# Optimization experiments

Measured on AMD Instinct MI355X. Metric: run time of the kernel, lower is better.

The kernel has to match this reference:

```python
import jax, jax.numpy as jnp
import numpy as np

N = 80000      # rechits per event
K = 512        # max truth objects (t_idx in [-1, K))
C = 2          # n_ccoords
NCLS = 6       # pred_id width
Q_MIN = 0.1
S_B = 1.0
NOISE_SCALER = 1.0
BETA_LOSS_SCALE = 1.0
POTENTIAL_SCALING = 1.0
REPULSION_SCALING = 1.0
ENERGY_LOSS_WEIGHT = 1.0
POSITION_LOSS_WEIGHT = 1.0
TIMING_LOSS_WEIGHT = 1.0
CLASSIFICATION_LOSS_WEIGHT = 1.0
CC_DAMPING = 0.001
EPS = 1e-9


def huber(x, d):
    absx = jnp.abs(x)
    return jnp.where(absx < d, x ** 2, d ** 2 + 2.0 * d * (absx - d))


def softclip(x, startclipat):
    x = x / startclipat
    x = jnp.where(x > 1.0, jnp.log(x + 1.0), x)
    return x * startclipat


def calc_energy_weights(t_energy):
    lower_cut = 0.5
    w = jnp.where(t_energy > 10.0, 1.0, (t_energy - lower_cut) / 10.0 * 10.0 / (10.0 - lower_cut))
    return jax.nn.relu(w)


def calc_energy_loss(t_energy, pred_energy):
    # alt_energy_loss=True branch: mild-gradient modified 1-exp form
    ediff = jnp.abs(t_energy - pred_energy)
    l = 10.0 * jnp.exp(-0.1 * ediff ** 2) + 0.01 * ediff
    return softclip(l, 10.0)


def calc_position_loss(t_pos, pred_pos):
    d2 = jnp.sum((t_pos - pred_pos) ** 2, axis=-1, keepdims=True)
    ploss = huber(jnp.sqrt(d2 / 10.0 ** 2 + 0.01), 10.0)
    return softclip(ploss, 3.0)


def calc_timing_loss(t_time, pred_time):
    return softclip(huber(t_time - pred_time, 2.0), 6.0)


def calc_classification_loss(t_pid, pred_id):
    return 1e-08 * jnp.mean(pred_id ** 2, axis=-1, keepdims=True)


def setup_inputs() -> dict:
    key = jax.random.key(0)
    ks = jax.random.split(key, 11)
    t_idx = jax.random.randint(ks[6], (N, 1), 0, K + 1) - 1  # -1 == noise
    return {
        'pred_beta': jax.random.uniform(ks[0], (N, 1), jnp.float32, 0.01, 0.99),
        'pred_ccoords': jax.random.normal(ks[1], (N, C), jnp.float32),
        'pred_energy': 100.0 * jax.random.uniform(ks[2], (N, 1), jnp.float32),
        'pred_pos': jax.random.normal(ks[3], (N, 2), jnp.float32),
        'pred_time': jax.random.normal(ks[4], (N, 1), jnp.float32),
        'pred_id': jax.random.normal(ks[5], (N, NCLS), jnp.float32),
        't_idx': t_idx.astype(jnp.int32),
        't_energy': 100.0 * jax.random.uniform(ks[7], (N, 1), jnp.float32),
        't_pos': jax.random.normal(ks[8], (N, 2), jnp.float32),
        't_time': jax.random.normal(ks[9], (N, 1), jnp.float32),
        't_pid': jax.random.uniform(ks[10], (N, 1), jnp.float32),
    }


def reference(pred_beta, pred_ccoords, pred_energy, pred_pos, pred_time, pred_id,
              t_idx, t_energy, t_pos, t_time, t_pid):
    beta = jnp.clip(pred_beta, 1e-6, 1.0 - 1e-6)                 # (N,1)
    q = jnp.arctanh(beta) ** 2 + Q_MIN                           # (N,1) charge

    is_obj = (t_idx >= 0)                                        # (N,1) bool
    M = (t_idx == jnp.arange(K)[None, :]) & is_obj               # (N,K) object membership
    Mf = M.astype(beta.dtype)
    obj_count = jnp.sum(Mf, axis=0)                              # (K,)
    has_obj = obj_count > 0.0                                    # (K,)
    n_obj = jnp.sum(has_obj.astype(beta.dtype)) + EPS

    # condensation point alpha_k: argmax beta within each object
    beta_masked = jnp.where(M, beta, -1.0)                       # (N,K)
    alpha = jnp.argmax(beta_masked, axis=0)                      # (K,)
    x_alpha = pred_ccoords[alpha]                                # (K,C)
    q_alpha = q[alpha, 0]                                        # (K,)
    beta_alpha = beta[alpha, 0]                                  # (K,)

    # pairwise squared distances hit <-> condensation point
    d2 = jnp.sum((pred_ccoords[:, None, :] - x_alpha[None, :, :]) ** 2, axis=-1)  # (N,K)

    # attractive potential (same object)
    att = Mf * d2 * q_alpha[None, :] * q                         # (N,K)
    L_att_k = jnp.sum(att, axis=0) / (obj_count + EPS)
    L_att = jnp.sum(jnp.where(has_obj, L_att_k, 0.0)) / n_obj

    # repulsive potential (other objects), hinge at unit distance
    rep = (1.0 - Mf) * jax.nn.relu(1.0 - jnp.sqrt(d2 + 1e-6)) * q_alpha[None, :] * q
    L_rep_k = jnp.sum(rep, axis=0) / (jnp.float32(N) - obj_count + EPS)
    L_rep = jnp.sum(jnp.where(has_obj, L_rep_k, 0.0)) / n_obj

    # beta loss: push condensation betas to 1, noise betas to 0
    L_beta = BETA_LOSS_SCALE * jnp.sum(jnp.where(has_obj, 1.0 - beta_alpha, 0.0)) / n_obj
    is_noise = (~is_obj).astype(beta.dtype)                      # (N,1)
    L_noise = S_B * NOISE_SCALER * jnp.sum(is_noise * beta) / (jnp.sum(is_noise) + EPS)

    # payload losses, beta- and energy-weighted, normalized per object
    payload = (ENERGY_LOSS_WEIGHT * calc_energy_loss(t_energy, pred_energy)
               + POSITION_LOSS_WEIGHT * calc_position_loss(t_pos, pred_pos)
               + TIMING_LOSS_WEIGHT * calc_timing_loss(t_time, pred_time)
               + CLASSIFICATION_LOSS_WEIGHT * calc_classification_loss(t_pid, pred_id))  # (N,1)
    pw = beta * calc_energy_weights(t_energy) * is_obj.astype(beta.dtype)               # (N,1)
    num = jnp.sum(Mf * (payload * pw), axis=0)                   # (K,)
    den = jnp.sum(Mf * pw, axis=0)                               # (K,)
    L_pay = jnp.sum(jnp.where(has_obj, num / (den + EPS), 0.0)) / n_obj

    L_cc = CC_DAMPING * jnp.mean(pred_ccoords ** 2)

    total = (POTENTIAL_SCALING * L_att + REPULSION_SCALING * L_rep
             + L_beta + L_noise + L_pay + L_cc)
    return total
```

## Files before the change

kernel.cpp:

```cpp
#include <hip/hip_runtime.h>
#include <math.h>

#define KOBJ  512
#define NCLS  6
#define QMIN  0.1f
#define EPSF  1e-9f

#define NBH  80
#define ROWS_PER (NBH / 16)
#define KC   64
#define GX   64
#define NTB  (GX * (KOBJ / KC))
#define HP   5

struct Ws {
    unsigned long long p_packed[NBH][KOBJ];
    float p_num[NBH][KOBJ];
    float p_den[NBH][KOBJ];
    int   p_cnt[NBH][KOBJ];
    float pnoise[NBH][4];
    float kvec[KOBJ * 4];
    float pobj[8][4];
    float pattrep[NTB][2];
};

__device__ __forceinline__ float clipb(float b) {
    return fminf(fmaxf(b, 1e-6f), 1.0f - 1e-6f);
}

__device__ __forceinline__ float fsqrt(float x)  { return __builtin_amdgcn_sqrtf(x); }
__device__ __forceinline__ float frcp(float x)   { return __builtin_amdgcn_rcpf(x); }
__device__ __forceinline__ float qval(float b) {
    float at = 0.5f * __logf((1.f + b) * frcp(1.f - b));
    return at * at + QMIN;
}

__device__ __forceinline__ float waveSum(float v) {
#pragma unroll
    for (int o = 32; o > 0; o >>= 1) v += __shfl_down(v, o, 64);
    return v;
}

__global__ __launch_bounds__(1024)
void k_hits(const float* __restrict__ beta_in, const float* __restrict__ cc,
            const float* __restrict__ pe,  const float* __restrict__ ppos,
            const float* __restrict__ pt,  const float* __restrict__ pid,
            const int*   __restrict__ tidx,const float* __restrict__ te,
            const float* __restrict__ tpos,const float* __restrict__ tt,
            Ws* __restrict__ ws, int n)
{
    const int b = blockIdx.x, t = threadIdx.x;

    __shared__ unsigned long long lpk[KOBJ];
    __shared__ float lnum[KOBJ], lden[KOBJ];
    __shared__ int   lcnt[KOBJ];
    for (int k = t; k < KOBJ; k += 1024) { lpk[k] = 0ull; lnum[k] = 0.f; lden[k] = 0.f; lcnt[k] = 0; }
    __syncthreads();

    float ccs = 0.f, nb = 0.f, nc = 0.f;
    const int i = b * 1024 + t;
    if (i < n) {
        float bb = clipb(beta_in[i]);
        float c0 = cc[2*i], c1 = cc[2*i+1];
        ccs = c0*c0 + c1*c1;
        int k = tidx[i];
        if (k >= 0) {
            unsigned long long key =
                ((unsigned long long)__float_as_uint(bb) << 32) | (unsigned)(~i);
            atomicMax(&lpk[k], key);
            atomicAdd(&lcnt[k], 1);

            float tei   = te[i];
            float ediff = fabsf(tei - pe[i]);
            float el = 10.f * __expf(-0.1f * ediff * ediff) + 0.01f * ediff;
            { float x = el * 0.1f; if (x > 1.f) x = __logf(x + 1.f); el = x * 10.f; }

            float dx  = tpos[2*i]   - ppos[2*i];
            float dy  = tpos[2*i+1] - ppos[2*i+1];
            float d2p = dx*dx + dy*dy;
            float hx  = fsqrt(d2p * 0.01f + 0.01f);
            float pl  = (hx < 10.f) ? hx*hx : 100.f + 20.f*(hx - 10.f);
            { float x = pl * (1.f/3.f); if (x > 1.f) x = __logf(x + 1.f); pl = x * 3.f; }

            float td  = tt[i] - pt[i];
            float atd = fabsf(td);
            float tl  = (atd < 2.f) ? td*td : 4.f + 4.f*(atd - 2.f);
            { float x = tl * (1.f/6.f); if (x > 1.f) x = __logf(x + 1.f); tl = x * 6.f; }

            float cls = 0.f;
#pragma unroll
            for (int j = 0; j < NCLS; ++j) { float v = pid[i*NCLS + j]; cls += v*v; }
            cls *= (1e-8f / (float)NCLS);

            float payload = el + pl + tl + cls;
            float ew = (tei > 10.f) ? 1.f : (tei - 0.5f) * (1.f / 9.5f);
            ew = fmaxf(ew, 0.f);
            float pw = bb * ew;
            atomicAdd(&lnum[k], payload * pw);
            atomicAdd(&lden[k], pw);
        } else {
            nb = bb; nc = 1.f;
        }
    }
    __syncthreads();

    if (t < KOBJ) {
        ws->p_packed[b][t] = lpk[t];
        ws->p_num[b][t]    = lnum[t];
        ws->p_den[b][t]    = lden[t];
        ws->p_cnt[b][t]    = lcnt[t];
    }

    __shared__ float sred[3][16];
    float A = waveSum(ccs), B = waveSum(nb), C = waveSum(nc);
    int lane = t & 63, wv = t >> 6;
    if (lane == 0) { sred[0][wv] = A; sred[1][wv] = B; sred[2][wv] = C; }
    __syncthreads();
    if (t == 0) {
        float a = 0.f, x = 0.f, y = 0.f;
        for (int j = 0; j < 16; ++j) { a += sred[0][j]; x += sred[1][j]; y += sred[2][j]; }
        ws->pnoise[b][0] = a; ws->pnoise[b][1] = x; ws->pnoise[b][2] = y;
    }
}

__global__ __launch_bounds__(1024)
void k_obj(const float* __restrict__ beta_in, const float* __restrict__ cc,
           Ws* __restrict__ ws, int n)
{
    const int t = threadIdx.x, lane = t & 63, wv = t >> 6;
    const int k = blockIdx.x * 64 + lane;

    unsigned long long pk = 0ull;
    float nm = 0.f, dn = 0.f;
    int   ct = 0;
#pragma unroll
    for (int j = wv * ROWS_PER; j < (wv + 1) * ROWS_PER; ++j) {
        unsigned long long v = ws->p_packed[j][k];
        pk = (v > pk) ? v : pk;
        nm += ws->p_num[j][k];
        dn += ws->p_den[j][k];
        ct += ws->p_cnt[j][k];
    }
    __shared__ unsigned long long spk[16][64];
    __shared__ float snum[16][64], sden[16][64];
    __shared__ int   scnt[16][64];
    spk[wv][lane] = pk; snum[wv][lane] = nm; sden[wv][lane] = dn; scnt[wv][lane] = ct;
    __syncthreads();

    if (wv == 0) {
#pragma unroll
        for (int j = 1; j < 16; ++j) {
            unsigned long long v = spk[j][lane];
            pk = (v > pk) ? v : pk;
            nm += snum[j][lane]; dn += sden[j][lane]; ct += scnt[j][lane];
        }
        float flag = 0.f, bsum = 0.f, payk = 0.f;
        float q_a = 0.f, x0 = 0.f, x1 = 0.f;
        if (ct > 0) {
            flag = 1.f;
            unsigned idx = ~(unsigned)(pk & 0xffffffffull);
            float bb = clipb(beta_in[idx]);
            bsum = 1.f - bb;
            q_a = qval(bb);
            x0 = cc[2*idx]; x1 = cc[2*idx + 1];
            payk = nm / (dn + EPSF);
        }
        ((float4*)ws->kvec)[k] = make_float4(
            x0, x1,
            flag * q_a / ((float)n - (float)ct + EPSF),
            flag * q_a / ((float)ct + EPSF));
        float f  = waveSum(flag);
        float bs = waveSum(bsum);
        float ps = waveSum(payk);
        if (lane == 0) {
            ws->pobj[blockIdx.x][0] = f;
            ws->pobj[blockIdx.x][1] = bs;
            ws->pobj[blockIdx.x][2] = ps;
        }
    }
}

__global__ __launch_bounds__(256)
void k_pair(const float* __restrict__ beta_in, const float* __restrict__ cc,
            const int* __restrict__ tidx, Ws* __restrict__ ws, int n)
{
    const int b = blockIdx.x, t = threadIdx.x;
    const int lane = t & 63, wv = t >> 6;
    const int kchunk = b / GX;
    const int xi     = b - kchunk * GX;
    const int kbase  = kchunk * KC;

    __shared__ float4 sk[KC];
    if (t < KC) sk[t] = ((const float4*)ws->kvec)[kbase + t];

    const int xspan = GX * 256;
    const int i0 = xi * 256 + t;
    float c0[HP], c1[HP], qq[HP], acc[HP];
    int   k0[HP];
#pragma unroll
    for (int j = 0; j < HP; ++j) {
        int i = i0 + j * xspan;
        bool v = (i < n);
        c0[j] = v ? cc[2*i]     : 1e30f;
        c1[j] = v ? cc[2*i + 1] : 1e30f;
        float bb = v ? clipb(beta_in[i]) : 0.5f;
        qq[j] = qval(bb);
        k0[j] = v ? tidx[i] : -1;
        acc[j] = 0.f;
    }
    __syncthreads();

#pragma unroll 4
    for (int k = 0; k < KC; ++k) {
        float4 kv = sk[k];
#pragma unroll
        for (int j = 0; j < HP; ++j) {
            float dx = c0[j] - kv.x, dy = c1[j] - kv.y;
            float d2e = fmaf(dx, dx, fmaf(dy, dy, 1e-6f));
            float r   = fsqrt(d2e);
            acc[j] = fmaf(fmaxf(1.f - r, 0.f), kv.z, acc[j]);
        }
    }

    float att = 0.f, rep = 0.f;
#pragma unroll
    for (int j = 0; j < HP; ++j) {
        int kk = k0[j] - kbase;
        if (kk >= 0 && kk < KC) {
            float4 kv = sk[kk];
            float dx = c0[j] - kv.x, dy = c1[j] - kv.y;
            float d2e = fmaf(dx, dx, fmaf(dy, dy, 1e-6f));
            float r   = fsqrt(d2e);
            acc[j] -= fmaxf(1.f - r, 0.f) * kv.z;
            float d2 = fmaf(dx, dx, dy * dy);
            att = fmaf(d2 * kv.w, qq[j], att);
        }
        rep = fmaf(acc[j], qq[j], rep);
    }

    __shared__ float sred[2][4];
    float A = waveSum(att), R = waveSum(rep);
    if (lane == 0) { sred[0][wv] = A; sred[1][wv] = R; }
    __syncthreads();
    if (t == 0) {
        float sa = 0.f, sr = 0.f;
        for (int j = 0; j < 4; ++j) { sa += sred[0][j]; sr += sred[1][j]; }
        ws->pattrep[b][0] = sa;
        ws->pattrep[b][1] = sr;
    }
}

__global__ __launch_bounds__(512)
void k_final(Ws* __restrict__ ws, float* __restrict__ out, int n)
{
    const int t = threadIdx.x, lane = t & 63, wv = t >> 6;

    float att = ws->pattrep[t][0];
    float rep = ws->pattrep[t][1];
    float ccs = 0.f, nB = 0.f, nC = 0.f;
    if (t < NBH) { ccs = ws->pnoise[t][0]; nB = ws->pnoise[t][1]; nC = ws->pnoise[t][2]; }
    float fS = 0.f, bS = 0.f, pS = 0.f;
    if (t < 8)   { fS = ws->pobj[t][0]; bS = ws->pobj[t][1]; pS = ws->pobj[t][2]; }

    att = waveSum(att); rep = waveSum(rep);
    ccs = waveSum(ccs); nB = waveSum(nB); nC = waveSum(nC);
    fS = waveSum(fS); bS = waveSum(bS); pS = waveSum(pS);

    __shared__ float fin[8][8];
    if (lane == 0) {
        fin[0][wv] = att; fin[1][wv] = rep; fin[2][wv] = ccs; fin[3][wv] = nB;
        fin[4][wv] = nC;  fin[5][wv] = fS;  fin[6][wv] = bS;  fin[7][wv] = pS;
    }
    __syncthreads();
    if (t == 0) {
        float v[8];
        for (int m = 0; m < 8; ++m) {
            v[m] = 0.f;
            for (int j = 0; j < 8; ++j) v[m] += fin[m][j];
        }
        float n_obj = v[5] + EPSF;
        out[0] = (v[0] + v[1] + v[6] + v[7]) / n_obj
               + v[3] / (v[4] + EPSF)
               + 0.001f * v[2] / (float)(2 * n);
    }
}

extern "C" void kernel_launch(void* const* d_in, const int* in_sizes, int n_in,
                              void* d_out, int out_size, void* d_ws, size_t ws_size,
                              hipStream_t stream)
{
    const float* pred_beta    = (const float*)d_in[0];
    const float* pred_ccoords = (const float*)d_in[1];
    const float* pred_energy  = (const float*)d_in[2];
    const float* pred_pos     = (const float*)d_in[3];
    const float* pred_time    = (const float*)d_in[4];
    const float* pred_id      = (const float*)d_in[5];
    const int*   t_idx        = (const int*)d_in[6];
    const float* t_energy     = (const float*)d_in[7];
    const float* t_pos        = (const float*)d_in[8];
    const float* t_time       = (const float*)d_in[9];

    float* out = (float*)d_out;
    Ws* ws = (Ws*)d_ws;
    int n = in_sizes[0];

    k_hits<<<NBH, 1024, 0, stream>>>(pred_beta, pred_ccoords, pred_energy, pred_pos,
                                     pred_time, pred_id, t_idx, t_energy, t_pos,
                                     t_time, ws, n);
    k_obj<<<8, 1024, 0, stream>>>(pred_beta, pred_ccoords, ws, n);
    k_pair<<<NTB, 256, 0, stream>>>(pred_beta, pred_ccoords, t_idx, ws, n);
    k_final<<<1, 512, 0, stream>>>(ws, out, n);
}
```

Measured before the change: 103.5 us.

## Fuse per-object reduction into pair kernel, removing separate k_obj launch

Removes the k_obj kernel and has each k_pair block redundantly reduce the per-hit-block partials for its own 64-object chunk, building the object vector directly in shared memory. Only the first x-block of each chunk writes the per-object sums. This saves one kernel launch and the global round-trip of kvec. In exchange, each of the 64 blocks per chunk re-reads 80 rows of partials, which adds L2 traffic and extra latency before the pair loop starts.

After: 99.45 us. -3.9%, faster.

```diff
diff --git a/kernel.cpp b/kernel.cpp
--- a/kernel.cpp
+++ b/kernel.cpp
@@ -7,11 +7,11 @@
 #define EPSF  1e-9f
 
 #define NBH  80
-#define ROWS_PER (NBH / 16)
 #define KC   64
 #define GX   64
 #define NTB  (GX * (KOBJ / KC))
 #define HP   5
+#define AROWS (NBH / 4)
 
 struct Ws {
     unsigned long long p_packed[NBH][KOBJ];
@@ -19,8 +19,7 @@
     float p_den[NBH][KOBJ];
     int   p_cnt[NBH][KOBJ];
     float pnoise[NBH][4];
-    float kvec[KOBJ * 4];
-    float pobj[8][4];
+    float pobj[KOBJ / KC][4];
     float pattrep[NTB][2];
 };
 
@@ -123,33 +122,55 @@
     }
 }
 
-__global__ __launch_bounds__(1024)
-void k_obj(const float* __restrict__ beta_in, const float* __restrict__ cc,
-           Ws* __restrict__ ws, int n)
+__global__ __launch_bounds__(256)
+void k_pair(const float* __restrict__ beta_in, const float* __restrict__ cc,
+            const int* __restrict__ tidx, Ws* __restrict__ ws, int n)
 {
-    const int t = threadIdx.x, lane = t & 63, wv = t >> 6;
-    const int k = blockIdx.x * 64 + lane;
-
-    unsigned long long pk = 0ull;
-    float nm = 0.f, dn = 0.f;
-    int   ct = 0;
-#pragma unroll
-    for (int j = wv * ROWS_PER; j < (wv + 1) * ROWS_PER; ++j) {
-        unsigned long long v = ws->p_packed[j][k];
-        pk = (v > pk) ? v : pk;
-        nm += ws->p_num[j][k];
-        dn += ws->p_den[j][k];
-        ct += ws->p_cnt[j][k];
-    }
-    __shared__ unsigned long long spk[16][64];
-    __shared__ float snum[16][64], sden[16][64];
-    __shared__ int   scnt[16][64];
-    spk[wv][lane] = pk; snum[wv][lane] = nm; sden[wv][lane] = dn; scnt[wv][lane] = ct;
-    __syncthreads();
-
+    const int b = blockIdx.x, t = threadIdx.x;
+    const int lane = t & 63, wv = t >> 6;
+    const int kchunk = b / GX;
+    const int xi     = b - kchunk * GX;
+    const int kbase  = kchunk * KC;
+
+    const int xspan = GX * 256;
+    const int i0 = xi * 256 + t;
+    float c0[HP], c1[HP], bH[HP];
+    int   k0[HP];
+#pragma unroll
+    for (int j = 0; j < HP; ++j) {
+        int i = i0 + j * xspan;
+        bool v = (i < n);
+        c0[j] = v ? cc[2*i]     : 1e30f;
+        c1[j] = v ? cc[2*i + 1] : 1e30f;
+        bH[j] = v ? beta_in[i]  : 0.5f;
+        k0[j] = v ? tidx[i] : -1;
+    }
+
+    __shared__ float4 sk[KC];
+    __shared__ unsigned long long spk[4][KC];
+    __shared__ float snum[4][KC], sden[4][KC];
+    __shared__ int   scnt[4][KC];
+    {
+        int k = kbase + lane;
+        unsigned long long pk = 0ull;
+        float nm = 0.f, dn = 0.f; int ct = 0;
+#pragma unroll 4
+        for (int j = wv * AROWS; j < (wv + 1) * AROWS; ++j) {
+            unsigned long long v = ws->p_packed[j][k];
+            pk = (v > pk) ? v : pk;
+            nm += ws->p_num[j][k];
+            dn += ws->p_den[j][k];
+            ct += ws->p_cnt[j][k];
+        }
+        spk[wv][lane] = pk; snum[wv][lane] = nm; sden[wv][lane] = dn; scnt[wv][lane] = ct;
+    }
+    __syncthreads();
     if (wv == 0) {
-#pragma unroll
-        for (int j = 1; j < 16; ++j) {
+        unsigned long long pk = spk[0][lane];
+        float nm = snum[0][lane], dn = sden[0][lane];
+        int ct = scnt[0][lane];
+#pragma unroll
+        for (int j = 1; j < 4; ++j) {
             unsigned long long v = spk[j][lane];
             pk = (v > pk) ? v : pk;
             nm += snum[j][lane]; dn += sden[j][lane]; ct += scnt[j][lane];
@@ -165,50 +186,28 @@
             x0 = cc[2*idx]; x1 = cc[2*idx + 1];
             payk = nm / (dn + EPSF);
         }
-        ((float4*)ws->kvec)[k] = make_float4(
-            x0, x1,
-            flag * q_a / ((float)n - (float)ct + EPSF),
-            flag * q_a / ((float)ct + EPSF));
-        float f  = waveSum(flag);
-        float bs = waveSum(bsum);
-        float ps = waveSum(payk);
-        if (lane == 0) {
-            ws->pobj[blockIdx.x][0] = f;
-            ws->pobj[blockIdx.x][1] = bs;
-            ws->pobj[blockIdx.x][2] = ps;
-        }
-    }
-}
-
-__global__ __launch_bounds__(256)
-void k_pair(const float* __restrict__ beta_in, const float* __restrict__ cc,
-            const int* __restrict__ tidx, Ws* __restrict__ ws, int n)
-{
-    const int b = blockIdx.x, t = threadIdx.x;
-    const int lane = t & 63, wv = t >> 6;
-    const int kchunk = b / GX;
-    const int xi     = b - kchunk * GX;
-    const int kbase  = kchunk * KC;
-
-    __shared__ float4 sk[KC];
-    if (t < KC) sk[t] = ((const float4*)ws->kvec)[kbase + t];
-
-    const int xspan = GX * 256;
-    const int i0 = xi * 256 + t;
-    float c0[HP], c1[HP], qq[HP], acc[HP];
-    int   k0[HP];
+        sk[lane] = make_float4(x0, x1,
+                               flag * q_a / ((float)n - (float)ct + EPSF),
+                               flag * q_a / ((float)ct + EPSF));
+        if (xi == 0) {
+            float f  = waveSum(flag);
+            float bs = waveSum(bsum);
+            float ps = waveSum(payk);
+            if (lane == 0) {
+                ws->pobj[kchunk][0] = f;
+                ws->pobj[kchunk][1] = bs;
+                ws->pobj[kchunk][2] = ps;
+            }
+        }
+    }
+    __syncthreads();
+
+    float qq[HP], acc[HP];
 #pragma unroll
     for (int j = 0; j < HP; ++j) {
-        int i = i0 + j * xspan;
-        bool v = (i < n);
-        c0[j] = v ? cc[2*i]     : 1e30f;
-        c1[j] = v ? cc[2*i + 1] : 1e30f;
-        float bb = v ? clipb(beta_in[i]) : 0.5f;
-        qq[j] = qval(bb);
-        k0[j] = v ? tidx[i] : -1;
+        qq[j] = qval(clipb(bH[j]));
         acc[j] = 0.f;
     }
-    __syncthreads();
 
 #pragma unroll 4
     for (int k = 0; k < KC; ++k) {
@@ -260,7 +259,7 @@
     float ccs = 0.f, nB = 0.f, nC = 0.f;
     if (t < NBH) { ccs = ws->pnoise[t][0]; nB = ws->pnoise[t][1]; nC = ws->pnoise[t][2]; }
     float fS = 0.f, bS = 0.f, pS = 0.f;
-    if (t < 8)   { fS = ws->pobj[t][0]; bS = ws->pobj[t][1]; pS = ws->pobj[t][2]; }
+    if (t < KOBJ / KC) { fS = ws->pobj[t][0]; bS = ws->pobj[t][1]; pS = ws->pobj[t][2]; }
 
     att = waveSum(att); rep = waveSum(rep);
     ccs = waveSum(ccs); nB = waveSum(nB); nC = waveSum(nC);
@@ -307,7 +306,6 @@
     k_hits<<<NBH, 1024, 0, stream>>>(pred_beta, pred_ccoords, pred_energy, pred_pos,
                                      pred_time, pred_id, t_idx, t_energy, t_pos,
                                      t_time, ws, n);
-    k_obj<<<8, 1024, 0, stream>>>(pred_beta, pred_ccoords, ws, n);
     k_pair<<<NTB, 256, 0, stream>>>(pred_beta, pred_ccoords, t_idx, ws, n);
     k_final<<<1, 512, 0, stream>>>(ws, out, n);
 }
```
